# Kernel tuning notes

Hardware: AMD Instinct MI355X
Metric: run time of the kernel (lower is better)

Reference implementation:

```python
import jax, jax.numpy as jnp
import numpy as np

D_MODEL = 1024
HEAD_SIZE = 128
SCALE = float(np.sqrt(HEAD_SIZE))


def setup_inputs() -> dict:
    key = jax.random.key(0)
    kx, kq, kk, kv = jax.random.split(key, 4)
    B, T = 4, 4096
    x = jax.random.normal(kx, (B, T, D_MODEL), dtype=jnp.float32)
    # torch nn.Linear(d_model, head_size, bias=False) weight: [head_size, d_model]
    s = 1.0 / np.sqrt(D_MODEL)
    Wq = jax.random.uniform(kq, (HEAD_SIZE, D_MODEL), jnp.float32, -s, s)
    Wk = jax.random.uniform(kk, (HEAD_SIZE, D_MODEL), jnp.float32, -s, s)
    Wv = jax.random.uniform(kv, (HEAD_SIZE, D_MODEL), jnp.float32, -s, s)
    return {"x": x, "Wq": Wq, "Wk": Wk, "Wv": Wv}


def reference(x, Wq, Wk, Wv):
    B, T, C = x.shape
    q = jnp.einsum('btc,hc->bth', x, Wq)  # [B,T,hs]
    k = jnp.einsum('btc,hc->bth', x, Wk)
    v = jnp.einsum('btc,hc->bth', x, Wv)
    scores = jnp.einsum('bth,bsh->bts', q, k) / SCALE  # [B,T,T]
    causal = jnp.tril(jnp.ones((T, T), dtype=bool))
    scores = jnp.where(causal, scores, -jnp.inf)
    attn = jax.nn.softmax(scores, axis=-1)
    # dropout p=0.0 -> identity
    return jnp.einsum('bts,bsh->bth', attn, v)
```

## Files before the change

kernel.cpp:

```cpp
#include <hip/hip_runtime.h>


typedef __attribute__((ext_vector_type(8))) short short8;
typedef __attribute__((ext_vector_type(8))) unsigned short ushort8;
typedef __attribute__((ext_vector_type(4))) unsigned short ushort4v;
typedef __attribute__((ext_vector_type(4))) float f32x4;
typedef __attribute__((ext_vector_type(16))) float f32x16;
typedef __attribute__((ext_vector_type(4))) int int4v;
typedef unsigned int u32;
typedef unsigned short u16;

#define MFMA32(a, b, c) __builtin_amdgcn_mfma_f32_32x32x16_bf16((a), (b), (c), 0, 0, 0)
#define WAITVM0() asm volatile("s_waitcnt vmcnt(0)" ::: "memory")
#define NEG_INF (-1e30f)

#define CHUNK 10
#define PITEMS 119
#define NITEMS 476

__device__ __forceinline__ void gload16(const void* g, void* l) {
  __builtin_amdgcn_global_load_lds((const __attribute__((address_space(1))) u32*)g,
                                   (__attribute__((address_space(3))) u32*)l, 16, 0, 0);
}

__device__ __forceinline__ u16 f2bf(float f) {
  u32 u = __builtin_bit_cast(u32, f);
  u = u + 0x7FFFu + ((u >> 16) & 1u);
  return (u16)(u >> 16);
}

__device__ __forceinline__ u32 cvtpk(float lo, float hi) {
  u32 r;
  asm("v_cvt_pk_bf16_f32 %0, %1, %2" : "=v"(r) : "v"(lo), "v"(hi));
  return r;
}

__global__ __launch_bounds__(256) void wconv_kernel(const float* __restrict__ Wq,
                                                    const float* __restrict__ Wk,
                                                    const float* __restrict__ Wv,
                                                    u16* __restrict__ Wb) {
  int g = (blockIdx.x * 256 + threadIdx.x) * 8;
  const float* src;
  if (g < 131072)      src = Wq + g;
  else if (g < 262144) src = Wk + (g - 131072);
  else                 src = Wv + (g - 262144);
  float4 a = *(const float4*)src;
  float4 b = *(const float4*)(src + 4);
  ushort8 o;
  o[0] = f2bf(a.x); o[1] = f2bf(a.y); o[2] = f2bf(a.z); o[3] = f2bf(a.w);
  o[4] = f2bf(b.x); o[5] = f2bf(b.y); o[6] = f2bf(b.z); o[7] = f2bf(b.w);
  *(ushort8*)(Wb + g) = o;
}

#define QK_SCALE 0.127517446f

__global__ __launch_bounds__(512, 2) void qkv_proj_kernel(const float* __restrict__ x,
                                                          const u16* __restrict__ Wb,
                                                          u16* __restrict__ qout,
                                                          u16* __restrict__ kout,
                                                          u16* __restrict__ vtout) {
  __shared__ __align__(16) unsigned char Wlds[2][49152];
  __shared__ __align__(16) unsigned char Xlds[2][8192];
  const int tid = threadIdx.x;
  const int w = tid >> 6;
  const int l = tid & 63;
  const int h = l >> 5, n32 = l & 31;
  const int mh = w >> 2, ng = w & 3;
  const int m0 = (int)blockIdx.x * 64;

  const int xr = tid >> 3, xc = tid & 7;
  const float* xsrc = x + (size_t)(m0 + xr) * 1024 + xc * 8;
  unsigned char* const xw0 = (unsigned char*)Xlds[0] + xr * 128 + ((xc * 16) ^ ((xr & 7) << 4));
  unsigned char* const xw1 = (unsigned char*)Xlds[1] + xr * 128 + ((xc * 16) ^ ((xr & 7) << 4));

  f32x16 acc[3];
#pragma unroll
  for (int j = 0; j < 3; ++j)
#pragma unroll
    for (int r = 0; r < 16; ++r) acc[j][r] = 0.f;

#define STAGE_W(buf, ks)                                                       \
  {                                                                            \
    _Pragma("unroll") for (int c = 0; c < 6; ++c) {                            \
      int L = c * 512 + tid;                                                   \
      int row = L >> 3, chp = L & 7;                                           \
      int gch = chp ^ (row & 7);                                               \
      gload16((const char*)Wb + row * 2048 + (ks) * 128 + gch * 16,            \
              (unsigned char*)Wlds[buf] + c * 8192 + w * 1024);                \
    }                                                                          \
  }

  float4 xa = *(const float4*)(xsrc);
  float4 xb = *(const float4*)(xsrc + 4);
  STAGE_W(0, 0);

  const int am = mh * 32 + n32;
  const int asw = (am & 7) << 4;
  int cur = 0;

  for (int ks = 0; ks < 16; ++ks) {
    int4v xv;
    xv[0] = (int)cvtpk(xa.x, xa.y);
    xv[1] = (int)cvtpk(xa.z, xa.w);
    xv[2] = (int)cvtpk(xb.x, xb.y);
    xv[3] = (int)cvtpk(xb.z, xb.w);
    *(int4v*)(cur ? xw1 : xw0) = xv;
    __syncthreads();
    if (ks < 15) {
      xa = *(const float4*)(xsrc + (ks + 1) * 64);
      xb = *(const float4*)(xsrc + (ks + 1) * 64 + 4);
      STAGE_W(cur ^ 1, ks + 1);
    }
    const char* xb0 = (const char*)Xlds[cur];
    const char* wb0 = (const char*)Wlds[cur];
    __builtin_amdgcn_s_setprio(1);
#pragma unroll
    for (int k16 = 0; k16 < 4; ++k16) {
      short8 a = *(const short8*)(xb0 + am * 128 + ((k16 * 32 + h * 16) ^ asw));
#pragma unroll
      for (int j = 0; j < 3; ++j) {
        int nrow = (ng * 3 + j) * 32 + n32;
        short8 b = *(const short8*)(wb0 + nrow * 128 +
                                    ((k16 * 32 + h * 16) ^ ((nrow & 7) << 4)));
        acc[j] = MFMA32(a, b, acc[j]);
      }
    }
    __builtin_amdgcn_s_setprio(0);
    cur ^= 1;
  }
#undef STAGE_W

  const int m0e = m0 + mh * 32;
#pragma unroll
  for (int j = 0; j < 3; ++j) {
    int ti = ng * 3 + j;
    int gcol = ti * 32 + n32;
    if (ti < 4) {
#pragma unroll
      for (int r = 0; r < 16; ++r) {
        int row = m0e + (r & 3) + 8 * (r >> 2) + 4 * h;
        qout[(size_t)row * 128 + gcol] = f2bf(acc[j][r] * QK_SCALE);
      }
    } else if (ti < 8) {
#pragma unroll
      for (int r = 0; r < 16; ++r) {
        int row = m0e + (r & 3) + 8 * (r >> 2) + 4 * h;
        kout[(size_t)row * 128 + (gcol - 128)] = f2bf(acc[j][r]);
      }
    } else {
      int d = gcol - 256;
#pragma unroll
      for (int rq = 0; rq < 4; ++rq) {
        int t0 = m0e + rq * 8 + 4 * h;
        ushort4v o4;
#pragma unroll
        for (int i = 0; i < 4; ++i) o4[i] = f2bf(acc[j][rq * 4 + i]);
        *(ushort4v*)&vtout[(size_t)((t0 >> 12) * 128 + d) * 4096 + (t0 & 4095)] = o4;
      }
    }
  }
}

template <bool SPLIT>
__global__ __launch_bounds__(256, 2) void attn_kernel(const u16* __restrict__ qws,
                                                      const u16* __restrict__ kws,
                                                      const u16* __restrict__ vtws,
                                                      float* __restrict__ out,
                                                      float* __restrict__ opart,
                                                      float* __restrict__ mlpart) {
  __shared__ __align__(16) unsigned char Klds[2][16384];
  __shared__ __align__(16) unsigned char Vlds[2][16384];

  const int tid = threadIdx.x;
  const int w = tid >> 6;
  const int l = tid & 63;
  const int h = l >> 5, q32 = l & 31;

  int bi, qt, s_lo, s_hi, item;
  if constexpr (SPLIT) {
    item = (int)blockIdx.x;
    bi = item / PITEMS;
    int r = item - bi * PITEMS;
    int base = 0;
    qt = 0;
    while (true) {
      int cnt = (qt + 5) / 5;
      if (r < base + cnt) { break; }
      base += cnt;
      ++qt;
    }
    int cc = r - base;
    int nsteps = 2 * qt + 2;
    s_lo = cc * CHUNK;
    s_hi = (s_lo + CHUNK < nsteps) ? s_lo + CHUNK : nsteps;
  } else {
    item = 0;
    int tb = (int)blockIdx.x;
    bi = tb & 3;
    qt = 31 - (tb >> 2);
    s_lo = 0;
    s_hi = 2 * qt + 2;
  }

  const int q0w = qt * 128 + w * 32;
  const int qg = q0w + q32;
  const int grow = bi * 4096 + qg;
  const int ql = w * 32 + q32;

  short8 qf[8];
  const u16* qp = qws + (size_t)grow * 128 + h * 8;
#pragma unroll
  for (int ks = 0; ks < 8; ++ks) qf[ks] = *(const short8*)(qp + ks * 16);

  f32x16 ot[4];
#pragma unroll
  for (int dt = 0; dt < 4; ++dt)
#pragma unroll
    for (int r = 0; r < 16; ++r) ot[dt][r] = 0.f;
  float mreg = NEG_INF, lsum = 0.f;

  const char* kbatch = (const char*)kws + (size_t)bi * 4096 * 256;
  const char* vbatch = (const char*)vtws + (size_t)bi * 128 * 8192;

#define STAGE_KV(buf, kv0)                                                     \
  {                                                                            \
    _Pragma("unroll") for (int c = 0; c < 4; ++c) {                            \
      int L = c * 256 + tid;                                                   \
      int row = L >> 4, chp = L & 15;                                          \
      int gch = chp ^ (row & 7);                                               \
      gload16(kbatch + (size_t)((kv0) + row) * 256 + gch * 16,                 \
              (unsigned char*)Klds[buf] + c * 4096 + w * 1024);                \
    }                                                                          \
    _Pragma("unroll") for (int c = 0; c < 4; ++c) {                            \
      int L = c * 256 + tid;                                                   \
      int row = L >> 3, chp = L & 7;                                           \
      int gch = chp ^ (row & 7);                                               \
      gload16(vbatch + (size_t)row * 8192 + (size_t)(kv0) * 2 + gch * 16,      \
              (unsigned char*)Vlds[buf] + c * 4096 + w * 1024);                \
    }                                                                          \
  }

  STAGE_KV(0, s_lo * 64);
  int cur = 0;

  for (int s = s_lo; s < s_hi; ++s) {
    WAITVM0();
    __builtin_amdgcn_s_barrier();
    __builtin_amdgcn_sched_barrier(0);
    if (s + 1 < s_hi) STAGE_KV(cur ^ 1, (s + 1) * 64);
    const int kv0 = s * 64;
    const bool active = (kv0 <= q0w + 31);

    if (active) {
      f32x16 st0, st1;
#pragma unroll
      for (int r = 0; r < 16; ++r) { st0[r] = 0.f; st1[r] = 0.f; }
      const char* Kb = (const char*)Klds[cur];
      const int sw = (q32 & 7) << 4;
      __builtin_amdgcn_s_setprio(1);
#pragma unroll
      for (int ks = 0; ks < 8; ++ks) {
        int coff = ks * 32 + h * 16;
        short8 a0 = *(const short8*)(Kb + q32 * 256 + (coff ^ sw));
        st0 = MFMA32(a0, qf[ks], st0);
        short8 a1 = *(const short8*)(Kb + (32 + q32) * 256 + (coff ^ sw));
        st1 = MFMA32(a1, qf[ks], st1);
      }
      __builtin_amdgcn_s_setprio(0);

      if (kv0 + 63 > q0w) {
#pragma unroll
        for (int r = 0; r < 16; ++r) {
          int kvr = kv0 + (r & 3) + 8 * (r >> 2) + 4 * h;
          if (kvr > qg) st0[r] = NEG_INF;
          if (kvr + 32 > qg) st1[r] = NEG_INF;
        }
      }

      float tmax = st0[0];
#pragma unroll
      for (int r = 1; r < 16; ++r) tmax = fmaxf(tmax, st0[r]);
#pragma unroll
      for (int r = 0; r < 16; ++r) tmax = fmaxf(tmax, st1[r]);
      tmax = fmaxf(tmax, __shfl_xor(tmax, 32));
      if (!__all(tmax <= mreg + 8.0f)) {
        float mnew = fmaxf(mreg, tmax);
        float alpha = exp2f(mreg - mnew);
        lsum *= alpha;
#pragma unroll
        for (int dt = 0; dt < 4; ++dt)
#pragma unroll
          for (int r = 0; r < 16; ++r) ot[dt][r] *= alpha;
        mreg = mnew;
      }
      float rs = 0.f;
#pragma unroll
      for (int r = 0; r < 16; ++r) { st0[r] = exp2f(st0[r] - mreg); rs += st0[r]; }
#pragma unroll
      for (int r = 0; r < 16; ++r) { st1[r] = exp2f(st1[r] - mreg); rs += st1[r]; }
      rs += __shfl_xor(rs, 32);
      lsum += rs;

      const char* Vb = (const char*)Vlds[cur];
      __builtin_amdgcn_s_setprio(1);
#pragma unroll
      for (int t = 0; t < 4; ++t) {
        const f32x16& stt = (t < 2) ? st0 : st1;
        const int rb = (t & 1) * 8;
        u32 A0 = cvtpk(stt[rb + 0], stt[rb + 1]);
        u32 C0 = cvtpk(stt[rb + 2], stt[rb + 3]);
        u32 B0 = cvtpk(stt[rb + 4], stt[rb + 5]);
        u32 D0 = cvtpk(stt[rb + 6], stt[rb + 7]);
        u32 Ax = (u32)__shfl_xor((int)A0, 32);
        u32 Bx = (u32)__shfl_xor((int)B0, 32);
        u32 Cx = (u32)__shfl_xor((int)C0, 32);
        u32 Dx = (u32)__shfl_xor((int)D0, 32);
        int4v pbv;
        pbv[0] = (int)(h ? Bx : A0);
        pbv[1] = (int)(h ? Dx : C0);
        pbv[2] = (int)(h ? B0 : Ax);
        pbv[3] = (int)(h ? D0 : Cx);
        short8 pb = __builtin_bit_cast(short8, pbv);
#pragma unroll
        for (int dt = 0; dt < 4; ++dt) {
          int row = dt * 32 + q32;
          short8 va = *(const short8*)(Vb + row * 128 + ((t * 32 + h * 16) ^ sw));
          ot[dt] = MFMA32(va, pb, ot[dt]);
        }
      }
      __builtin_amdgcn_s_setprio(0);
    }
    cur ^= 1;
  }

  if constexpr (!SPLIT) {
    float inv = 1.0f / lsum;
    float* ob = out + (size_t)grow * 128;
#pragma unroll
    for (int dt = 0; dt < 4; ++dt)
#pragma unroll
      for (int rq = 0; rq < 4; ++rq) {
        f32x4 v4;
#pragma unroll
        for (int i = 0; i < 4; ++i) v4[i] = ot[dt][rq * 4 + i] * inv;
        *(f32x4*)(ob + dt * 32 + rq * 8 + 4 * h) = v4;
      }
  } else {
    float* ob = opart + (size_t)item * 16384 + (size_t)ql * 128;
#pragma unroll
    for (int dt = 0; dt < 4; ++dt)
#pragma unroll
      for (int rq = 0; rq < 4; ++rq) {
        f32x4 v4;
#pragma unroll
        for (int i = 0; i < 4; ++i) v4[i] = ot[dt][rq * 4 + i];
        *(f32x4*)(ob + dt * 32 + rq * 8 + 4 * h) = v4;
      }
    if (h == 0) {
      mlpart[item * 128 + ql] = mreg;
      mlpart[NITEMS * 128 + item * 128 + ql] = lsum;
    }
  }
#undef STAGE_KV
}

__global__ __launch_bounds__(256) void combine_kernel(const float* __restrict__ opart,
                                                      const float* __restrict__ mlpart,
                                                      float* __restrict__ out) {
  int idx = blockIdx.x * 256 + threadIdx.x;
  int row = idx >> 7, d = idx & 127;
  int bi = row >> 12, lrow = row & 4095;
  int qt = lrow >> 7, ql = lrow & 127;
  int base = 0;
#pragma unroll 1
  for (int j = 0; j < qt; ++j) base += (j + 5) / 5;
  int nspl = (qt + 5) / 5;
  int it0 = bi * PITEMS + base;

  float M = NEG_INF;
#pragma unroll 1
  for (int j = 0; j < nspl; ++j)
    M = fmaxf(M, mlpart[(it0 + j) * 128 + ql]);
  float L = 0.f, O = 0.f;
#pragma unroll 1
  for (int j = 0; j < nspl; ++j) {
    float s = exp2f(mlpart[(it0 + j) * 128 + ql] - M);
    L += mlpart[NITEMS * 128 + (it0 + j) * 128 + ql] * s;
    O += opart[(size_t)(it0 + j) * 16384 + (size_t)ql * 128 + d] * s;
  }
  out[(size_t)row * 128 + d] = O / L;
}

extern "C" void kernel_launch(void* const* d_in, const int* in_sizes, int n_in,
                              void* d_out, int out_size, void* d_ws, size_t ws_size,
                              hipStream_t stream) {
  (void)in_sizes; (void)n_in; (void)out_size;
  const float* x  = (const float*)d_in[0];
  const float* Wq = (const float*)d_in[1];
  const float* Wk = (const float*)d_in[2];
  const float* Wv = (const float*)d_in[3];
  float* out = (float*)d_out;
  char* ws = (char*)d_ws;
  u16* qws  = (u16*)(ws);
  u16* kws  = (u16*)(ws + (4u << 20));
  u16* vtws = (u16*)(ws + (8u << 20));
  u16* Wb   = (u16*)(ws + (12u << 20));
  float* opart  = (float*)(ws + (13u << 20));
  float* mlpart = (float*)(ws + (47u << 20));

  wconv_kernel<<<dim3(192), dim3(256), 0, stream>>>(Wq, Wk, Wv, Wb);
  qkv_proj_kernel<<<dim3(256), dim3(512), 0, stream>>>(x, Wb, qws, kws, vtws);
  if (ws_size >= ((size_t)48 << 20)) {
    attn_kernel<true><<<dim3(NITEMS), dim3(256), 0, stream>>>(qws, kws, vtws, nullptr, opart, mlpart);
    combine_kernel<<<dim3(8192), dim3(256), 0, stream>>>(opart, mlpart, out);
  } else {
    attn_kernel<false><<<dim3(128), dim3(256), 0, stream>>>(qws, kws, vtws, out, nullptr, nullptr);
  }
}
```

Measured before the change: 92.62 us.

## Split QKV projection output columns across two blocks per row tile

The QKV projection now launches 512 blocks of 256 threads instead of 256 blocks of 512. Each block computes half of the 384 output columns (selected by blockIdx>>8) for a 64-row tile, which halves the weight LDS footprint per block. The intent is to fill more CUs on a 256-CU part with smaller blocks and allow higher occupancy. In exchange, every x row tile is loaded and converted twice, raising global traffic for x.

```diff
diff --git a/kernel.cpp b/kernel.cpp
--- a/kernel.cpp
+++ b/kernel.cpp
@@ -7,6 +7,7 @@
 typedef __attribute__((ext_vector_type(4))) float f32x4;
 typedef __attribute__((ext_vector_type(16))) float f32x16;
 typedef __attribute__((ext_vector_type(4))) int int4v;
+typedef __attribute__((ext_vector_type(2))) unsigned int u32x2;
 typedef unsigned int u32;
 typedef unsigned short u16;
 
@@ -54,24 +55,28 @@
 
 #define QK_SCALE 0.127517446f
 
-__global__ __launch_bounds__(512, 2) void qkv_proj_kernel(const float* __restrict__ x,
+__global__ __launch_bounds__(256, 2) void qkv_proj_kernel(const float* __restrict__ x,
                                                           const u16* __restrict__ Wb,
                                                           u16* __restrict__ qout,
                                                           u16* __restrict__ kout,
                                                           u16* __restrict__ vtout) {
-  __shared__ __align__(16) unsigned char Wlds[2][49152];
+  __shared__ __align__(16) unsigned char Wlds[2][24576];
   __shared__ __align__(16) unsigned char Xlds[2][8192];
   const int tid = threadIdx.x;
   const int w = tid >> 6;
   const int l = tid & 63;
   const int h = l >> 5, n32 = l & 31;
-  const int mh = w >> 2, ng = w & 3;
-  const int m0 = (int)blockIdx.x * 64;
-
-  const int xr = tid >> 3, xc = tid & 7;
-  const float* xsrc = x + (size_t)(m0 + xr) * 1024 + xc * 8;
-  unsigned char* const xw0 = (unsigned char*)Xlds[0] + xr * 128 + ((xc * 16) ^ ((xr & 7) << 4));
-  unsigned char* const xw1 = (unsigned char*)Xlds[1] + xr * 128 + ((xc * 16) ^ ((xr & 7) << 4));
+  const int mh = w >> 1, ng = w & 1;
+  const int bx = (int)blockIdx.x;
+  const int ns = bx >> 8;
+  const int m0 = (bx & 255) * 64;
+
+  const int xr = tid >> 2, xc = tid & 3;
+  const float* xsrc = x + (size_t)(m0 + xr) * 1024 + xc * 16;
+  const int xsw = (xr & 7) << 4;
+  unsigned char* const xw[2] = {
+    (unsigned char*)Xlds[0] + xr * 128,
+    (unsigned char*)Xlds[1] + xr * 128};
 
   f32x16 acc[3];
 #pragma unroll
@@ -82,16 +87,29 @@
 #define STAGE_W(buf, ks)                                                       \
   {                                                                            \
     _Pragma("unroll") for (int c = 0; c < 6; ++c) {                            \
-      int L = c * 512 + tid;                                                   \
+      int L = c * 256 + tid;                                                   \
       int row = L >> 3, chp = L & 7;                                           \
       int gch = chp ^ (row & 7);                                               \
-      gload16((const char*)Wb + row * 2048 + (ks) * 128 + gch * 16,            \
-              (unsigned char*)Wlds[buf] + c * 8192 + w * 1024);                \
+      gload16((const char*)Wb + (size_t)(ns * 192 + row) * 2048 + (ks) * 128 + \
+                  gch * 16,                                                    \
+              (unsigned char*)Wlds[buf] + c * 4096 + w * 1024);                \
     }                                                                          \
   }
-
-  float4 xa = *(const float4*)(xsrc);
-  float4 xb = *(const float4*)(xsrc + 4);
+#define WRITE_X(buf)                                                           \
+  {                                                                            \
+    int4v p0, p1;                                                              \
+    p0[0] = (int)cvtpk(xa0.x, xa0.y); p0[1] = (int)cvtpk(xa0.z, xa0.w);        \
+    p0[2] = (int)cvtpk(xa1.x, xa1.y); p0[3] = (int)cvtpk(xa1.z, xa1.w);        \
+    p1[0] = (int)cvtpk(xa2.x, xa2.y); p1[1] = (int)cvtpk(xa2.z, xa2.w);        \
+    p1[2] = (int)cvtpk(xa3.x, xa3.y); p1[3] = (int)cvtpk(xa3.z, xa3.w);        \
+    *(int4v*)(xw[buf] + ((xc * 32) ^ xsw)) = p0;                               \
+    *(int4v*)(xw[buf] + ((xc * 32 + 16) ^ xsw)) = p1;                          \
+  }
+
+  float4 xa0 = *(const float4*)(xsrc);
+  float4 xa1 = *(const float4*)(xsrc + 4);
+  float4 xa2 = *(const float4*)(xsrc + 8);
+  float4 xa3 = *(const float4*)(xsrc + 12);
   STAGE_W(0, 0);
 
   const int am = mh * 32 + n32;
@@ -99,16 +117,13 @@
   int cur = 0;
 
   for (int ks = 0; ks < 16; ++ks) {
-    int4v xv;
-    xv[0] = (int)cvtpk(xa.x, xa.y);
-    xv[1] = (int)cvtpk(xa.z, xa.w);
-    xv[2] = (int)cvtpk(xb.x, xb.y);
-    xv[3] = (int)cvtpk(xb.z, xb.w);
-    *(int4v*)(cur ? xw1 : xw0) = xv;
+    WRITE_X(cur);
     __syncthreads();
     if (ks < 15) {
-      xa = *(const float4*)(xsrc + (ks + 1) * 64);
-      xb = *(const float4*)(xsrc + (ks + 1) * 64 + 4);
+      xa0 = *(const float4*)(xsrc + (ks + 1) * 64);
+      xa1 = *(const float4*)(xsrc + (ks + 1) * 64 + 4);
+      xa2 = *(const float4*)(xsrc + (ks + 1) * 64 + 8);
+      xa3 = *(const float4*)(xsrc + (ks + 1) * 64 + 12);
       STAGE_W(cur ^ 1, ks + 1);
     }
     const char* xb0 = (const char*)Xlds[cur];
@@ -129,19 +144,20 @@
     cur ^= 1;
   }
 #undef STAGE_W
+#undef WRITE_X
 
   const int m0e = m0 + mh * 32;
 #pragma unroll
   for (int j = 0; j < 3; ++j) {
-    int ti = ng * 3 + j;
-    int gcol = ti * 32 + n32;
-    if (ti < 4) {
+    int tig = ns * 6 + ng * 3 + j;
+    int gcol = tig * 32 + n32;
+    if (tig < 4) {
 #pragma unroll
       for (int r = 0; r < 16; ++r) {
         int row = m0e + (r & 3) + 8 * (r >> 2) + 4 * h;
         qout[(size_t)row * 128 + gcol] = f2bf(acc[j][r] * QK_SCALE);
       }
-    } else if (ti < 8) {
+    } else if (tig < 8) {
 #pragma unroll
       for (int r = 0; r < 16; ++r) {
         int row = m0e + (r & 3) + 8 * (r >> 2) + 4 * h;
@@ -409,7 +425,7 @@
   float* mlpart = (float*)(ws + (47u << 20));
 
   wconv_kernel<<<dim3(192), dim3(256), 0, stream>>>(Wq, Wk, Wv, Wb);
-  qkv_proj_kernel<<<dim3(256), dim3(512), 0, stream>>>(x, Wb, qws, kws, vtws);
+  qkv_proj_kernel<<<dim3(512), dim3(256), 0, stream>>>(x, Wb, qws, kws, vtws);
   if (ws_size >= ((size_t)48 << 20)) {
     attn_kernel<true><<<dim3(NITEMS), dim3(256), 0, stream>>>(qws, kws, vtws, nullptr, opart, mlpart);
     combine_kernel<<<dim3(8192), dim3(256), 0, stream>>>(opart, mlpart, out);
```

Result: no change. 91.02 us (-1.7%).
